# Optimization experiments

Measured on AMD Instinct MI355X. Metric: run time of the kernel, lower is better.

The kernel has to match this reference:

```python
import jax, jax.numpy as jnp
import numpy as np

N, E, K, C, NB, G = 10000, 320000, 10, 32, 8, 8
RMAX, AVG = 5.0, 32.0
L_OF_M = np.array([0,1,1,1,2,2,2,2,2,3,3,3,3,3,3,3])
BLOCKS = [(0,1),(1,4),(4,9),(9,16)]


def _sph(u):
    # real spherical harmonics l=0..3, e3nn 'component' normalization (sum_m Y_lm^2 = 2l+1)
    x, y, z = u[:,0], u[:,1], u[:,2]
    s3=3**0.5; s5=5**0.5; s15=15**0.5; s105=105**0.5
    s35_8=(35.0/8.0)**0.5; s21_8=(21.0/8.0)**0.5; s7=7**0.5
    return jnp.stack([
        jnp.ones_like(x),
        s3*x, s3*y, s3*z,
        s15*x*y, s15*y*z, 0.5*s5*(3*z*z-1.0), s15*x*z, 0.5*s15*(x*x-y*y),
        s35_8*y*(3*x*x-y*y), s105*x*y*z, s21_8*y*(5*z*z-1.0),
        0.5*s7*z*(5*z*z-3.0), s21_8*x*(5*z*z-1.0), 0.5*s105*z*(x*x-y*y),
        s35_8*x*(x*x-3*y*y)], axis=-1)


def _radial(r):
    # Bessel basis * polynomial cutoff (p=5)
    n = jnp.arange(1, NB+1, dtype=r.dtype)
    bess = jnp.sqrt(2.0/RMAX)*jnp.sin(n*jnp.pi*r[:,None]/RMAX)/r[:,None]
    t = r/RMAX; p = 5.0
    env = 1.0 - (p+1)*(p+2)/2*t**5 + p*(p+2)*t**6 - p*(p+1)/2*t**7
    env = jnp.where(r < RMAX, env, 0.0)
    return bess*env[:,None]


def _interact(scal, ea, ef, snd, rcv, mws, Wl, n_nodes):
    h = ef
    for W in mws[:-1]:
        h = jax.nn.silu(h @ W)
    tw = (h @ mws[-1]).reshape(-1, C, 4)[:, :, L_OF_M]          # [E,C,16] per-(channel,l) tp weights
    mji = scal[snd][:, :, None] * tw * ea[:, None, :]            # per-edge CG-style tensor product
    msg = jax.ops.segment_sum(mji, rcv, num_segments=n_nodes) / AVG
    return jnp.concatenate([jnp.einsum('ncm,cd->ndm', msg[:, :, a:b], Wl[l])
                            for l, (a, b) in enumerate(BLOCKS)], axis=-1)


def _forward(positions, node_attrs, shifts, edge_index, batch, num_graphs,
             atomic_energies, W_emb, Wup1, M1a, M1b, M1c, M1d, Wl1, Wprod1,
             Wup2, M2a, M2b, M2c, M2d, Wl2, Wprod2, Wsc2, wr1, Wr2a, wr2b):
    snd, rcv = edge_index[0], edge_index[1]
    vec = positions[rcv] - positions[snd] + shifts
    r = jnp.sqrt(jnp.sum(vec*vec, -1) + 1e-12)
    ea = _sph(vec / r[:, None])           # [E,16]
    ef = _radial(r)                       # [E,8]
    nf0 = node_attrs @ W_emb              # node embedding [N,C]
    A1 = _interact(nf0 @ Wup1, ea, ef, snd, rcv, (M1a, M1b, M1c, M1d), Wl1, positions.shape[0])
    c1 = jnp.einsum('nk,kct->nct', node_attrs, Wprod1)          # element-dep product-basis coeffs
    a0 = A1[:, :, 0]
    nf1 = A1 * (c1[..., 0] + c1[..., 1]*a0 + c1[..., 2]*a0*a0)[:, :, None]  # correlation-3 product
    A2 = _interact(nf1[:, :, 0] @ Wup2, ea, ef, snd, rcv, (M2a, M2b, M2c, M2d), Wl2, positions.shape[0])
    pl = jnp.stack([jnp.sum(A2[:, :, a:b]**2, -1) for a, b in BLOCKS], -1)  # [N,C,4] invariants
    c2 = jnp.einsum('nk,kct->nct', node_attrs, Wprod2)
    nf2 = jnp.sum(c2*pl, -1) + jnp.einsum('nk,nc,kcd->nd', node_attrs, nf1[:, :, 0], Wsc2)
    e0 = node_attrs @ atomic_energies
    e1 = nf1[:, :, 0] @ wr1
    e2 = jax.nn.silu(nf2 @ Wr2a) @ wr2b
    node_energy = e0 + e1 + e2
    total = jax.ops.segment_sum(node_energy, batch, num_segments=num_graphs)
    return total, node_energy


def setup_inputs():
    key = jax.random.key(0)
    ks = jax.random.split(key, 24)
    s = 0.1
    inp = {}
    inp['positions'] = jax.random.normal(ks[0], (N, 3), jnp.float32)
    inp['node_attrs'] = jax.nn.one_hot(jax.random.randint(ks[1], (N,), 0, K), K, dtype=jnp.float32)
    inp['shifts'] = jnp.zeros((E, 3), jnp.float32)
    inp['edge_index'] = jax.random.randint(ks[2], (2, E), 0, N)
    inp['batch'] = jnp.sort(jax.random.randint(ks[3], (N,), 0, G))
    inp['num_graphs'] = G
    inp['atomic_energies'] = jax.random.normal(ks[4], (K,), jnp.float32)
    inp['W_emb'] = s*jax.random.normal(ks[5], (K, C), jnp.float32)
    inp['Wup1'] = s*jax.random.normal(ks[6], (C, C), jnp.float32)
    inp['M1a'] = s*jax.random.normal(ks[7], (NB, 64), jnp.float32)
    inp['M1b'] = s*jax.random.normal(ks[8], (64, 64), jnp.float32)
    inp['M1c'] = s*jax.random.normal(ks[9], (64, 64), jnp.float32)
    inp['M1d'] = s*jax.random.normal(ks[10], (64, C*4), jnp.float32)
    inp['Wl1'] = s*jax.random.normal(ks[11], (4, C, C), jnp.float32)
    inp['Wprod1'] = s*jax.random.normal(ks[12], (K, C, 3), jnp.float32)
    inp['Wup2'] = s*jax.random.normal(ks[13], (C, C), jnp.float32)
    inp['M2a'] = s*jax.random.normal(ks[14], (NB, 64), jnp.float32)
    inp['M2b'] = s*jax.random.normal(ks[15], (64, 64), jnp.float32)
    inp['M2c'] = s*jax.random.normal(ks[16], (64, 64), jnp.float32)
    inp['M2d'] = s*jax.random.normal(ks[17], (64, C*4), jnp.float32)
    inp['Wl2'] = s*jax.random.normal(ks[18], (4, C, C), jnp.float32)
    inp['Wprod2'] = s*jax.random.normal(ks[19], (K, C, 4), jnp.float32)
    inp['Wsc2'] = s*jax.random.normal(ks[20], (K, C, C), jnp.float32)
    inp['wr1'] = s*jax.random.normal(ks[21], (C,), jnp.float32)
    inp['Wr2a'] = s*jax.random.normal(ks[22], (C, 16), jnp.float32)
    inp['wr2b'] = s*jax.random.normal(ks[23], (16,), jnp.float32)
    return inp


def reference(positions, node_attrs, shifts, edge_index, batch, num_graphs,
              atomic_energies, W_emb, Wup1, M1a, M1b, M1c, M1d, Wl1, Wprod1,
              Wup2, M2a, M2b, M2c, M2d, Wl2, Wprod2, Wsc2, wr1, Wr2a, wr2b):
    def efn(pos):
        tot, ne = _forward(pos, node_attrs, shifts, edge_index, batch, num_graphs,
                           atomic_energies, W_emb, Wup1, M1a, M1b, M1c, M1d, Wl1, Wprod1,
                           Wup2, M2a, M2b, M2c, M2d, Wl2, Wprod2, Wsc2, wr1, Wr2a, wr2b)
        return jnp.sum(tot), (tot, ne)
    (_, (total, node_energy)), g = jax.value_and_grad(efn, has_aux=True)(positions)
    forces = -g  # forces = -dE/dpositions as in get_outputs
    return total, node_energy, forces
```

## Files before the change

### kernel.cpp

```cpp
#include <hip/hip_runtime.h>
#include <math.h>

#define NN 10000
#define NE 320000
#define KS 10
#define CC 32
#define GG 8
#define NTAB 4096
#define TROW 320
#define RMAXf 5.0f
#define AVGf 32.0f

#define OF_TAB 0
#define SZ_TAB ((NTAB + 1) * TROW)
#define OF_SC1 (OF_TAB + SZ_TAB)
#define OF_SP (OF_SC1 + KS * CC)
#define OF_RE (OF_SP + NN)
#define OF_UE (OF_RE + NE)
#define OF_GV (OF_UE + 3 * NE)
#define OF_A0 (OF_GV + 3 * NE)
#define OF_NF1 (OF_A0 + NN * CC)
#define OF_SCAL2 (OF_NF1 + NN * CC)
#define OF_NEP (OF_SCAL2 + NN * CC)
#define OF_GM2T (OF_NEP + NN)
#define OF_GNF1P (OF_GM2T + NN * CC * 16)
#define OF_GS1 (OF_GNF1P + NN * CC)
#define OF_ROWS (OF_GS1 + NN * CC)
#define OF_ELIST (OF_ROWS + NN + 1)
#define OF_DEG (OF_ELIST + NE)
#define OF_CUR (OF_DEG + NN)
#define OF_GSC2 (OF_CUR + NN)
#define OF_END (OF_GSC2 + NN * CC)

__device__ __forceinline__ int lm_of(int m) { return (m == 0) ? 0 : (m < 4) ? 1 : (m < 9) ? 2 : 3; }

__device__ __forceinline__ void sph16(float x, float y, float z, float* Y) {
    const float s3 = 1.7320508075688772f, s5 = 2.23606797749979f, s15 = 3.872983346207417f,
                s105 = 10.246950765959598f, s358 = 2.091650066335189f,
                s218 = 1.6201851746019651f, s7 = 2.6457513110645907f;
    Y[0] = 1.f;
    Y[1] = s3 * x; Y[2] = s3 * y; Y[3] = s3 * z;
    Y[4] = s15 * x * y; Y[5] = s15 * y * z; Y[6] = 0.5f * s5 * (3.f * z * z - 1.f);
    Y[7] = s15 * x * z; Y[8] = 0.5f * s15 * (x * x - y * y);
    Y[9] = s358 * y * (3.f * x * x - y * y);
    Y[10] = s105 * x * y * z;
    Y[11] = s218 * y * (5.f * z * z - 1.f);
    Y[12] = 0.5f * s7 * z * (5.f * z * z - 3.f);
    Y[13] = s218 * x * (5.f * z * z - 1.f);
    Y[14] = 0.5f * s105 * z * (x * x - y * y);
    Y[15] = s358 * x * (x * x - 3.f * y * y);
}

__device__ __forceinline__ void sph16_grad(float x, float y, float z, float* Dx, float* Dy, float* Dz) {
    const float s3 = 1.7320508075688772f, s5 = 2.23606797749979f, s15 = 3.872983346207417f,
                s105 = 10.246950765959598f, s358 = 2.091650066335189f,
                s218 = 1.6201851746019651f, s7 = 2.6457513110645907f;
    Dx[0] = 0; Dy[0] = 0; Dz[0] = 0;
    Dx[1] = s3; Dy[1] = 0; Dz[1] = 0;
    Dx[2] = 0; Dy[2] = s3; Dz[2] = 0;
    Dx[3] = 0; Dy[3] = 0; Dz[3] = s3;
    Dx[4] = s15 * y; Dy[4] = s15 * x; Dz[4] = 0;
    Dx[5] = 0; Dy[5] = s15 * z; Dz[5] = s15 * y;
    Dx[6] = 0; Dy[6] = 0; Dz[6] = 3.f * s5 * z;
    Dx[7] = s15 * z; Dy[7] = 0; Dz[7] = s15 * x;
    Dx[8] = s15 * x; Dy[8] = -s15 * y; Dz[8] = 0;
    Dx[9] = 6.f * s358 * x * y; Dy[9] = 3.f * s358 * (x * x - y * y); Dz[9] = 0;
    Dx[10] = s105 * y * z; Dy[10] = s105 * x * z; Dz[10] = s105 * x * y;
    Dx[11] = 0; Dy[11] = s218 * (5.f * z * z - 1.f); Dz[11] = 10.f * s218 * y * z;
    Dx[12] = 0; Dy[12] = 0; Dz[12] = 0.5f * s7 * (15.f * z * z - 3.f);
    Dx[13] = s218 * (5.f * z * z - 1.f); Dy[13] = 0; Dz[13] = 10.f * s218 * x * z;
    Dx[14] = s105 * x * z; Dy[14] = -s105 * y * z; Dz[14] = 0.5f * s105 * (x * x - y * y);
    Dx[15] = 3.f * s358 * (x * x - y * y); Dy[15] = -6.f * s358 * x * y; Dz[15] = 0;
}

__global__ void k_species(const float* __restrict__ na, int* __restrict__ sp) {
    int n = blockIdx.x * blockDim.x + threadIdx.x;
    if (n >= NN) return;
    int k = 0;
    for (int j = 0; j < KS; j++)
        if (na[n * KS + j] > 0.5f) k = j;
    sp[n] = k;
}

__global__ void k_scal1(const float* __restrict__ Wemb, const float* __restrict__ Wup1, float* __restrict__ st) {
    int i = threadIdx.x;
    if (i >= KS * CC) return;
    int k = i / CC, c = i % CC;
    float s = 0;
    for (int j = 0; j < CC; j++) s += Wemb[k * CC + j] * Wup1[j * CC + c];
    st[i] = s;
}

__global__ void k_table(const float* __restrict__ M1a, const float* __restrict__ M1b,
                        const float* __restrict__ M1c, const float* __restrict__ M1d,
                        const float* __restrict__ M2a, const float* __restrict__ M2b,
                        const float* __restrict__ M2c, const float* __restrict__ M2d,
                        float* __restrict__ tab) {
    const double PI = 3.14159265358979323846;
    int row = blockIdx.x;
    int j = threadIdx.x;
    __shared__ float sR[8], sdR[8];
    __shared__ float sA[64], sdA[64], sB[64], sdB[64];
    if (j < 8) {
        double r = (double)row * ((double)RMAXf / NTAB);
        if (r < 1e-6) r = 1e-6;
        double a = (double)(j + 1) * PI / (double)RMAXf;
        double env = 0.0, denv = 0.0;
        if (row < NTAB) {
            double t = r / (double)RMAXf;
            double t4 = t * t * t * t;
            env = 1.0 - 21.0 * t4 * t + 35.0 * t4 * t * t - 15.0 * t4 * t * t * t;
            denv = (-105.0 * t4 + 210.0 * t4 * t - 105.0 * t4 * t * t) / (double)RMAXf;
        }
        double pref = sqrt(2.0 / (double)RMAXf);
        double s = sin(a * r), cg = cos(a * r);
        double bess = pref * s / r;
        double dbess = pref * (a * cg / r - s / (r * r));
        sR[j] = (float)(bess * env);
        sdR[j] = (float)(dbess * env + bess * denv);
    }
    __syncthreads();
    size_t rb = (size_t)row * TROW;

    {
        float p = 0, dp = 0;
        for (int i = 0; i < 8; i++) { float w = M1a[i * 64 + j]; p += sR[i] * w; dp += sdR[i] * w; }
        float sg = 1.f / (1.f + expf(-p));
        sB[j] = p * sg; sdB[j] = dp * sg * (1.f + p * (1.f - sg));
    }
    __syncthreads();
    {
        float p = 0, dp = 0;
        for (int i = 0; i < 64; i++) { float w = M1b[i * 64 + j]; p += sB[i] * w; dp += sdB[i] * w; }
        float sg = 1.f / (1.f + expf(-p));
        sA[j] = p * sg; sdA[j] = dp * sg * (1.f + p * (1.f - sg));
    }
    __syncthreads();
    {
        float p = 0, dp = 0;
        for (int i = 0; i < 64; i++) { float w = M1c[i * 64 + j]; p += sA[i] * w; dp += sdA[i] * w; }
        float sg = 1.f / (1.f + expf(-p));
        sB[j] = p * sg; sdB[j] = dp * sg * (1.f + p * (1.f - sg));
    }
    __syncthreads();
    #pragma unroll
    for (int t2 = 0; t2 < 2; t2++) {
        int o = j + t2 * 64;
        if ((o & 3) == 0) {
            float p = 0, dp = 0;
            for (int i = 0; i < 64; i++) { float w = M1d[i * 128 + o]; p += sB[i] * w; dp += sdB[i] * w; }
            int c = o >> 2;
            tab[rb + c] = p;
            tab[rb + 32 + c] = dp;
        }
    }
    __syncthreads();

    {
        float p = 0, dp = 0;
        for (int i = 0; i < 8; i++) { float w = M2a[i * 64 + j]; p += sR[i] * w; dp += sdR[i] * w; }
        float sg = 1.f / (1.f + expf(-p));
        sB[j] = p * sg; sdB[j] = dp * sg * (1.f + p * (1.f - sg));
    }
    __syncthreads();
    {
        float p = 0, dp = 0;
        for (int i = 0; i < 64; i++) { float w = M2b[i * 64 + j]; p += sB[i] * w; dp += sdB[i] * w; }
        float sg = 1.f / (1.f + expf(-p));
        sA[j] = p * sg; sdA[j] = dp * sg * (1.f + p * (1.f - sg));
    }
    __syncthreads();
    {
        float p = 0, dp = 0;
        for (int i = 0; i < 64; i++) { float w = M2c[i * 64 + j]; p += sA[i] * w; dp += sdA[i] * w; }
        float sg = 1.f / (1.f + expf(-p));
        sB[j] = p * sg; sdB[j] = dp * sg * (1.f + p * (1.f - sg));
    }
    __syncthreads();
    #pragma unroll
    for (int t2 = 0; t2 < 2; t2++) {
        int o = j + t2 * 64;
        float p = 0, dp = 0;
        for (int i = 0; i < 64; i++) { float w = M2d[i * 128 + o]; p += sB[i] * w; dp += sdB[i] * w; }
        tab[rb + 64 + o] = p;
        tab[rb + 192 + o] = dp;
    }
}

__global__ void k_geom(const float* __restrict__ pos, const float* __restrict__ shifts,
                       const int* __restrict__ ei, float* __restrict__ re,
                       float* __restrict__ ue, int* __restrict__ deg) {
    int e = blockIdx.x * 256 + threadIdx.x;
    if (e >= NE) return;
    int s = ei[e], t = ei[NE + e];
    float vx = pos[3 * t] - pos[3 * s] + shifts[3 * e];
    float vy = pos[3 * t + 1] - pos[3 * s + 1] + shifts[3 * e + 1];
    float vz = pos[3 * t + 2] - pos[3 * s + 2] + shifts[3 * e + 2];
    float r = sqrtf(vx * vx + vy * vy + vz * vz + 1e-12f);
    float inv = 1.f / r;
    re[e] = r;
    ue[3 * e] = vx * inv;
    ue[3 * e + 1] = vy * inv;
    ue[3 * e + 2] = vz * inv;
    atomicAdd(&deg[t], 1);
}

__global__ void k_scan(const int* __restrict__ deg, int* __restrict__ rows, int* __restrict__ cur) {
    __shared__ int part[1024];
    int t = threadIdx.x;
    const int per = (NN + 1023) / 1024;
    int base = t * per;
    int s = 0;
    for (int i = 0; i < per; i++) {
        int idx = base + i;
        if (idx < NN) s += deg[idx];
    }
    part[t] = s;
    __syncthreads();
    for (int off = 1; off < 1024; off <<= 1) {
        int v = (t >= off) ? part[t - off] : 0;
        __syncthreads();
        part[t] += v;
        __syncthreads();
    }
    int run = (t == 0) ? 0 : part[t - 1];
    for (int i = 0; i < per; i++) {
        int idx = base + i;
        if (idx < NN) {
            rows[idx] = run;
            cur[idx] = run;
            run += deg[idx];
        }
    }
    if (t == 1023) rows[NN] = run;
}

__global__ void k_fill(const int* __restrict__ ei, int* __restrict__ cur, int* __restrict__ elist) {
    int e = blockIdx.x * 256 + threadIdx.x;
    if (e >= NE) return;
    int t = ei[NE + e];
    int p = atomicAdd(&cur[t], 1);
    elist[p] = e;
}

__global__ void k_gather1(const int* __restrict__ rows, const int* __restrict__ elist,
                          const int* __restrict__ ei, const int* __restrict__ sp,
                          const float* __restrict__ re, const float* __restrict__ sc1,
                          const float* __restrict__ tab, const float* __restrict__ Wl1,
                          const float* __restrict__ Wprod1, const float* __restrict__ Wup2,
                          const float* __restrict__ wr1, const float* __restrict__ aE,
                          float* __restrict__ a0s, float* __restrict__ nf1,
                          float* __restrict__ scal2, float* __restrict__ nep) {
    int wid = (blockIdx.x * 256 + threadIdx.x) >> 6;
    int lane = threadIdx.x & 63, c = lane & 31, h = lane >> 5, hb = h << 5;
    if (wid >= NN) return;
    int r0 = rows[wid], dg = rows[wid + 1] - r0;
    float acc = 0.f;
    for (int j = h; j < dg; j += 2) {
        int e = elist[r0 + j];
        int s = ei[e];
        float r = re[e];
        float w1 = 0.f;
        if (r < RMAXf) {
            float tt = r * (NTAB / RMAXf);
            int i = (int)tt; if (i > NTAB - 1) i = NTAB - 1;
            float f = tt - (float)i;
            size_t b = (size_t)i * TROW + c;
            w1 = tab[b] * (1.f - f) + tab[b + TROW] * f;
        }
        acc += sc1[sp[s] * CC + c] * w1;
    }
    acc += __shfl_xor(acc, 32, 64);
    float a0 = 0.f;
    for (int d = 0; d < CC; d++) a0 += __shfl(acc, hb + d, 64) * Wl1[d * CC + c];
    a0 *= (1.f / AVGf);
    int k = sp[wid];
    const float* cp = &Wprod1[(k * CC + c) * 3];
    float nf = a0 * (cp[0] + cp[1] * a0 + cp[2] * a0 * a0);
    float s2 = 0.f;
    for (int d = 0; d < CC; d++) s2 += __shfl(nf, hb + d, 64) * Wup2[d * CC + c];
    float t1 = nf * wr1[c];
    for (int m = 16; m >= 1; m >>= 1) t1 += __shfl_xor(t1, m, 64);
    if (h == 0) {
        a0s[wid * CC + c] = a0;
        nf1[wid * CC + c] = nf;
        scal2[wid * CC + c] = s2;
        if (c == 0) nep[wid] = aE[k] + t1;
    }
}

__global__ void k_node2(const int* __restrict__ rows, const int* __restrict__ elist,
                        const int* __restrict__ ei, const int* __restrict__ sp,
                        const float* __restrict__ re, const float* __restrict__ ue,
                        const float* __restrict__ scal2, const float* __restrict__ tab,
                        const float* __restrict__ Wl2, const float* __restrict__ Wprod2,
                        const float* __restrict__ Wsc2, const float* __restrict__ nf1,
                        const float* __restrict__ Wr2a, const float* __restrict__ wr2b,
                        const float* __restrict__ wr1, const float* __restrict__ nep,
                        const int* __restrict__ batch,
                        float* __restrict__ gm2T, float* __restrict__ gnf1p,
                        float* __restrict__ out_total, float* __restrict__ out_ne) {
    __shared__ float lds[4][16 * 32];
    int wid = (blockIdx.x * 256 + threadIdx.x) >> 6;
    int lane = threadIdx.x & 63, c = lane & 31, h = lane >> 5, hb = h << 5;
    int w = threadIdx.x >> 6;
    if (wid >= NN) return;
    int r0 = rows[wid], dg = rows[wid + 1] - r0;
    float S2r[16];
    #pragma unroll
    for (int m = 0; m < 16; m++) S2r[m] = 0.f;
    for (int j = h; j < dg; j += 2) {
        int e = elist[r0 + j];
        int s = ei[e];
        float r = re[e];
        float w2[4] = {0, 0, 0, 0};
        if (r < RMAXf) {
            float tt = r * (NTAB / RMAXf);
            int i = (int)tt; if (i > NTAB - 1) i = NTAB - 1;
            float f = tt - (float)i;
            size_t b = (size_t)i * TROW + 64 + c * 4;
            #pragma unroll
            for (int l = 0; l < 4; l++) w2[l] = tab[b + l] * (1.f - f) + tab[b + TROW + l] * f;
        }
        float ux = ue[3 * e], uy = ue[3 * e + 1], uz = ue[3 * e + 2];
        float Y[16];
        sph16(ux, uy, uz, Y);
        float sc = scal2[s * CC + c];
        #pragma unroll
        for (int m = 0; m < 16; m++) S2r[m] += sc * w2[lm_of(m)] * Y[m];
    }
    #pragma unroll
    for (int m = 0; m < 16; m++) S2r[m] += __shfl_xor(S2r[m], 32, 64);
    if (h == 0) {
        #pragma unroll
        for (int m = 0; m < 16; m++) lds[w][m * 32 + c] = S2r[m];
    }
    __syncthreads();
    int d = c;
    float A2r[16];
    #pragma unroll
    for (int m = 0; m < 16; m++) {
        const float* wl = &Wl2[lm_of(m) * CC * CC];
        float acc = 0;
        for (int cc = 0; cc < CC; cc++) acc += lds[w][m * 32 + cc] * wl[cc * CC + d];
        A2r[m] = acc * (1.f / AVGf);
    }
    float pl[4] = {0, 0, 0, 0};
    #pragma unroll
    for (int m = 0; m < 16; m++) pl[lm_of(m)] += A2r[m] * A2r[m];
    int k = sp[wid];
    const float* c2 = &Wprod2[(k * CC + d) * 4];
    float nf2 = c2[0] * pl[0] + c2[1] * pl[1] + c2[2] * pl[2] + c2[3] * pl[3];
    for (int cc = 0; cc < CC; cc++) nf2 += nf1[wid * CC + cc] * Wsc2[((size_t)k * CC + cc) * CC + d];
    int jj = d & 15;
    float zj = 0;
    for (int dd = 0; dd < CC; dd++) zj += __shfl(nf2, hb + dd, 64) * Wr2a[dd * 16 + jj];
    float sg = 1.f / (1.f + expf(-zj));
    float e2p = (d < 16) ? zj * sg * wr2b[jj] : 0.f;
    float red = e2p;
    for (int m = 16; m >= 1; m >>= 1) red += __shfl_xor(red, m, 64);
    if (h == 0 && d == 0) {
        float ne = nep[wid] + red;
        out_ne[wid] = ne;
        atomicAdd(&out_total[batch[wid]], ne);
    }
    float gz = sg * (1.f + zj * (1.f - sg)) * wr2b[jj];
    float gn = 0;
    for (int j2 = 0; j2 < 16; j2++) gn += Wr2a[d * 16 + j2] * __shfl(gz, hb + j2, 64);
    __syncthreads();
    if (h == 0) {
        #pragma unroll
        for (int m = 0; m < 16; m++) lds[w][m * 32 + d] = 2.f * A2r[m] * gn * c2[lm_of(m)];
    }
    __syncthreads();
    float gmv[16];
    #pragma unroll
    for (int m = 0; m < 16; m++) {
        const float* wl = &Wl2[lm_of(m) * CC * CC + c * CC];
        float acc = 0;
        for (int dd = 0; dd < CC; dd++) acc += lds[w][m * 32 + dd] * wl[dd];
        gmv[m] = acc * (1.f / AVGf);
    }
    float g1 = wr1[c];
    for (int dd = 0; dd < CC; dd++) g1 += __shfl(gn, hb + dd, 64) * Wsc2[((size_t)k * CC + c) * CC + dd];
    if (h == 0) {
        #pragma unroll
        for (int m = 0; m < 16; m++) gm2T[(size_t)wid * 512 + c * 16 + m] = gmv[m];
        gnf1p[wid * CC + c] = g1;
    }
}

__global__ void k_gbwd2(const int* __restrict__ rows, const int* __restrict__ elist,
                        const int* __restrict__ ei, const float* __restrict__ re,
                        const float* __restrict__ ue, const float* __restrict__ scal2,
                        const float* __restrict__ tab, const float* __restrict__ gm2T,
                        float* __restrict__ gsc2, float* __restrict__ gvec) {
    int wid = (blockIdx.x * 256 + threadIdx.x) >> 6;
    int lane = threadIdx.x & 63, c = lane & 31, h = lane >> 5;
    if (wid >= NN) return;
    float gm[16];
    #pragma unroll
    for (int m = 0; m < 16; m++) gm[m] = gm2T[(size_t)wid * 512 + c * 16 + m];
    int r0 = rows[wid], dg = rows[wid + 1] - r0;
    for (int j = h; j < dg; j += 2) {
        int e = elist[r0 + j];
        int s = ei[e];
        float r = re[e];
        float w2[4] = {0, 0, 0, 0}, dw2[4] = {0, 0, 0, 0};
        if (r < RMAXf) {
            float tt = r * (NTAB / RMAXf);
            int i = (int)tt; if (i > NTAB - 1) i = NTAB - 1;
            float f = tt - (float)i;
            size_t b = (size_t)i * TROW + 64 + c * 4;
            size_t b2 = (size_t)i * TROW + 192 + c * 4;
            #pragma unroll
            for (int l = 0; l < 4; l++) {
                w2[l] = tab[b + l] * (1.f - f) + tab[b + TROW + l] * f;
                dw2[l] = tab[b2 + l] * (1.f - f) + tab[b2 + TROW + l] * f;
            }
        }
        float ux = ue[3 * e], uy = ue[3 * e + 1], uz = ue[3 * e + 2];
        float Y[16], Dx[16], Dy[16], Dz[16];
        sph16(ux, uy, uz, Y);
        sph16_grad(ux, uy, uz, Dx, Dy, Dz);
        float sc = scal2[s * CC + c];
        float gsc = 0, gdr = 0, gx = 0, gy = 0, gz = 0;
        #pragma unroll
        for (int m = 0; m < 16; m++) {
            float g = gm[m];
            int l = lm_of(m);
            float wv = w2[l];
            gsc += g * wv * Y[m];
            gdr += g * Y[m] * sc * dw2[l];
            float gY = g * sc * wv;
            gx += gY * Dx[m]; gy += gY * Dy[m]; gz += gY * Dz[m];
        }
        atomicAdd(&gsc2[s * CC + c], gsc);
        for (int m2 = 16; m2 >= 1; m2 >>= 1) {
            gdr += __shfl_xor(gdr, m2, 64);
            gx += __shfl_xor(gx, m2, 64);
            gy += __shfl_xor(gy, m2, 64);
            gz += __shfl_xor(gz, m2, 64);
        }
        if (c == 0) {
            float inv = 1.f / r;
            float dot = ux * gx + uy * gy + uz * gz;
            gvec[3 * e] = ux * gdr + (gx - ux * dot) * inv;
            gvec[3 * e + 1] = uy * gdr + (gy - uy * dot) * inv;
            gvec[3 * e + 2] = uz * gdr + (gz - uz * dot) * inv;
        }
    }
}

__global__ void k_node_bwd2(const float* __restrict__ gnf1p, const float* __restrict__ gsc2,
                            const float* __restrict__ Wup2, const float* __restrict__ a0s,
                            const int* __restrict__ sp, const float* __restrict__ Wprod1,
                            const float* __restrict__ Wl1, float* __restrict__ gS1) {
    int gid = blockIdx.x * 256 + threadIdx.x;
    int n = gid >> 5, c = gid & 31;
    if (n >= NN) return;
    int hb = threadIdx.x & 32;
    float g1 = gnf1p[n * CC + c];
    for (int dd = 0; dd < CC; dd++) g1 += gsc2[n * CC + dd] * Wup2[c * CC + dd];
    float a0 = a0s[n * CC + c];
    int k = sp[n];
    const float* cp = &Wprod1[(k * CC + c) * 3];
    float ga0 = g1 * (cp[0] + 2.f * cp[1] * a0 + 3.f * cp[2] * a0 * a0);
    float acc = 0;
    for (int dd = 0; dd < CC; dd++) acc += __shfl(ga0, hb + dd, 64) * Wl1[c * CC + dd];
    gS1[n * CC + c] = acc * (1.f / AVGf);
}

__global__ void k_edge_bwd1(const int* __restrict__ ei, const int* __restrict__ sp,
                            const float* __restrict__ re, const float* __restrict__ ue,
                            const float* __restrict__ sc1, const float* __restrict__ tab,
                            const float* __restrict__ gS1, const float* __restrict__ gvec,
                            float* __restrict__ F) {
    int gid = blockIdx.x * 256 + threadIdx.x;
    int e = gid >> 5, c = gid & 31;
    if (e >= NE) return;
    int s = ei[e], t = ei[NE + e];
    float r = re[e];
    float dw = 0.f;
    if (r < RMAXf) {
        float tt = r * (NTAB / RMAXf);
        int i = (int)tt; if (i > NTAB - 1) i = NTAB - 1;
        float f = tt - (float)i;
        size_t b = (size_t)i * TROW + 32 + c;
        dw = tab[b] * (1.f - f) + tab[b + TROW] * f;
    }
    float gw = gS1[t * CC + c] * sc1[sp[s] * CC + c];
    float gdr = gw * dw;
    for (int m = 16; m >= 1; m >>= 1) gdr += __shfl_xor(gdr, m, 64);
    if (c < 3) {
        float u = ue[3 * e + c];
        float gv = gvec[3 * e + c] + u * gdr;
        atomicAdd(&F[3 * s + c], gv);
        atomicAdd(&F[3 * t + c], -gv);
    }
}

extern "C" void kernel_launch(void* const* d_in, const int* in_sizes, int n_in,
                              void* d_out, int out_size, void* d_ws, size_t ws_size,
                              hipStream_t stream) {
    const float* pos = (const float*)d_in[0];
    const float* na = (const float*)d_in[1];
    const float* shifts = (const float*)d_in[2];
    const int* ei = (const int*)d_in[3];
    const int* batch = (const int*)d_in[4];
    const float* aE = (const float*)d_in[6];
    const float* Wemb = (const float*)d_in[7];
    const float* Wup1 = (const float*)d_in[8];
    const float* M1a = (const float*)d_in[9];
    const float* M1b = (const float*)d_in[10];
    const float* M1c = (const float*)d_in[11];
    const float* M1d = (const float*)d_in[12];
    const float* Wl1 = (const float*)d_in[13];
    const float* Wprod1 = (const float*)d_in[14];
    const float* Wup2 = (const float*)d_in[15];
    const float* M2a = (const float*)d_in[16];
    const float* M2b = (const float*)d_in[17];
    const float* M2c = (const float*)d_in[18];
    const float* M2d = (const float*)d_in[19];
    const float* Wl2 = (const float*)d_in[20];
    const float* Wprod2 = (const float*)d_in[21];
    const float* Wsc2 = (const float*)d_in[22];
    const float* wr1 = (const float*)d_in[23];
    const float* Wr2a = (const float*)d_in[24];
    const float* wr2b = (const float*)d_in[25];

    float* ws = (float*)d_ws;
    float* tab = ws + OF_TAB;
    float* sc1 = ws + OF_SC1;
    int* sp = (int*)(ws + OF_SP);
    float* re = ws + OF_RE;
    float* ue = ws + OF_UE;
    float* gv = ws + OF_GV;
    float* a0s = ws + OF_A0;
    float* nf1 = ws + OF_NF1;
    float* scal2 = ws + OF_SCAL2;
    float* nep = ws + OF_NEP;
    float* gm2T = ws + OF_GM2T;
    float* gnf1p = ws + OF_GNF1P;
    float* gS1 = ws + OF_GS1;
    int* rows = (int*)(ws + OF_ROWS);
    int* elist = (int*)(ws + OF_ELIST);
    int* deg = (int*)(ws + OF_DEG);
    int* cur = (int*)(ws + OF_CUR);
    float* gsc2 = ws + OF_GSC2;

    float* out_total = (float*)d_out;
    float* out_ne = out_total + GG;
    float* out_F = out_ne + NN;

    hipMemsetAsync(d_out, 0, sizeof(float) * (GG + NN + 3 * NN), stream);
    hipMemsetAsync(deg, 0, sizeof(float) * (size_t)(OF_END - OF_DEG), stream);

    k_species<<<(NN + 255) / 256, 256, 0, stream>>>(na, sp);
    k_scal1<<<1, 320, 0, stream>>>(Wemb, Wup1, sc1);
    k_table<<<NTAB + 1, 64, 0, stream>>>(M1a, M1b, M1c, M1d, M2a, M2b, M2c, M2d, tab);
    k_geom<<<(NE + 255) / 256, 256, 0, stream>>>(pos, shifts, ei, re, ue, deg);
    k_scan<<<1, 1024, 0, stream>>>(deg, rows, cur);
    k_fill<<<(NE + 255) / 256, 256, 0, stream>>>(ei, cur, elist);
    k_gather1<<<(NN + 3) / 4, 256, 0, stream>>>(rows, elist, ei, sp, re, sc1, tab, Wl1, Wprod1,
                                                Wup2, wr1, aE, a0s, nf1, scal2, nep);
    k_node2<<<(NN + 3) / 4, 256, 0, stream>>>(rows, elist, ei, sp, re, ue, scal2, tab, Wl2,
                                              Wprod2, Wsc2, nf1, Wr2a, wr2b, wr1, nep, batch,
                                              gm2T, gnf1p, out_total, out_ne);
    k_gbwd2<<<(NN + 3) / 4, 256, 0, stream>>>(rows, elist, ei, re, ue, scal2, tab, gm2T, gsc2, gv);
    k_node_bwd2<<<NN / 8, 256, 0, stream>>>(gnf1p, gsc2, Wup2, a0s, sp, Wprod1, Wl1, gS1);
    k_edge_bwd1<<<NE / 8, 256, 0, stream>>>(ei, sp, re, ue, sc1, tab, gS1, gv, out_F);
}
```

Measured before the change: 532.6 us.

## Store per-edge data in CSR order, unroll edge loops, fuse grad-backward into node2

k_fill now writes sender index, sender species and a packed float4 (r, unit vector) in receiver-sorted CSR order. The gather kernels then read contiguously instead of chasing elist/ei/re/ue indirections. The edge loops are unrolled 4x (2x in the backward) so several independent loads are in flight at once. The separate k_gbwd2 kernel is merged into k_node2, which removes the gm2T intermediate buffer's round trip and one launch. In exchange, k_fill does extra scattered writes and k_node2 gets more registers and lower occupancy.

```diff
diff --git a/kernel.cpp b/kernel.cpp
--- a/kernel.cpp
+++ b/kernel.cpp
@@ -13,7 +13,10 @@
 
 #define OF_TAB 0
 #define SZ_TAB ((NTAB + 1) * TROW)
-#define OF_SC1 (OF_TAB + SZ_TAB)
+#define OF_GEO (OF_TAB + SZ_TAB)
+#define OF_SND (OF_GEO + 4 * NE)
+#define OF_SPK (OF_SND + NE)
+#define OF_SC1 (OF_SPK + NE)
 #define OF_SP (OF_SC1 + KS * CC)
 #define OF_RE (OF_SP + NN)
 #define OF_UE (OF_RE + NE)
@@ -22,8 +25,7 @@
 #define OF_NF1 (OF_A0 + NN * CC)
 #define OF_SCAL2 (OF_NF1 + NN * CC)
 #define OF_NEP (OF_SCAL2 + NN * CC)
-#define OF_GM2T (OF_NEP + NN)
-#define OF_GNF1P (OF_GM2T + NN * CC * 16)
+#define OF_GNF1P (OF_NEP + NN)
 #define OF_GS1 (OF_GNF1P + NN * CC)
 #define OF_ROWS (OF_GS1 + NN * CC)
 #define OF_ELIST (OF_ROWS + NN + 1)
@@ -235,20 +237,26 @@
     if (t == 1023) rows[NN] = run;
 }
 
-__global__ void k_fill(const int* __restrict__ ei, int* __restrict__ cur, int* __restrict__ elist) {
+__global__ void k_fill(const int* __restrict__ ei, const int* __restrict__ sp,
+                       const float* __restrict__ re, const float* __restrict__ ue,
+                       int* __restrict__ cur, int* __restrict__ elist,
+                       int* __restrict__ snd, int* __restrict__ spk, float4* __restrict__ geo) {
     int e = blockIdx.x * 256 + threadIdx.x;
     if (e >= NE) return;
-    int t = ei[NE + e];
+    int s = ei[e], t = ei[NE + e];
     int p = atomicAdd(&cur[t], 1);
     elist[p] = e;
-}
-
-__global__ void k_gather1(const int* __restrict__ rows, const int* __restrict__ elist,
-                          const int* __restrict__ ei, const int* __restrict__ sp,
-                          const float* __restrict__ re, const float* __restrict__ sc1,
-                          const float* __restrict__ tab, const float* __restrict__ Wl1,
-                          const float* __restrict__ Wprod1, const float* __restrict__ Wup2,
-                          const float* __restrict__ wr1, const float* __restrict__ aE,
+    snd[p] = s;
+    spk[p] = sp[s];
+    geo[p] = make_float4(re[e], ue[3 * e], ue[3 * e + 1], ue[3 * e + 2]);
+}
+
+__global__ void k_gather1(const int* __restrict__ rows, const int* __restrict__ spk,
+                          const float4* __restrict__ geo, const int* __restrict__ sp,
+                          const float* __restrict__ sc1, const float* __restrict__ tab,
+                          const float* __restrict__ Wl1, const float* __restrict__ Wprod1,
+                          const float* __restrict__ Wup2, const float* __restrict__ wr1,
+                          const float* __restrict__ aE,
                           float* __restrict__ a0s, float* __restrict__ nf1,
                           float* __restrict__ scal2, float* __restrict__ nep) {
     int wid = (blockIdx.x * 256 + threadIdx.x) >> 6;
@@ -256,19 +264,30 @@
     if (wid >= NN) return;
     int r0 = rows[wid], dg = rows[wid + 1] - r0;
     float acc = 0.f;
-    for (int j = h; j < dg; j += 2) {
-        int e = elist[r0 + j];
-        int s = ei[e];
-        float r = re[e];
-        float w1 = 0.f;
-        if (r < RMAXf) {
-            float tt = r * (NTAB / RMAXf);
-            int i = (int)tt; if (i > NTAB - 1) i = NTAB - 1;
-            float f = tt - (float)i;
-            size_t b = (size_t)i * TROW + c;
-            w1 = tab[b] * (1.f - f) + tab[b + TROW] * f;
-        }
-        acc += sc1[sp[s] * CC + c] * w1;
+    for (int j = h; j < dg; j += 8) {
+        float rv[4]; int kv[4]; bool act[4];
+        #pragma unroll
+        for (int u = 0; u < 4; u++) {
+            int jj = j + 2 * u;
+            act[u] = jj < dg;
+            int p = r0 + (act[u] ? jj : 0);
+            rv[u] = geo[p].x;
+            kv[u] = spk[p];
+        }
+        #pragma unroll
+        for (int u = 0; u < 4; u++) {
+            if (!act[u]) continue;
+            float r = rv[u];
+            float w1 = 0.f;
+            if (r < RMAXf) {
+                float tt = r * (NTAB / RMAXf);
+                int i = (int)tt; if (i > NTAB - 1) i = NTAB - 1;
+                float f = tt - (float)i;
+                size_t b = (size_t)i * TROW + c;
+                w1 = tab[b] * (1.f - f) + tab[b + TROW] * f;
+            }
+            acc += sc1[kv[u] * CC + c] * w1;
+        }
     }
     acc += __shfl_xor(acc, 32, 64);
     float a0 = 0.f;
@@ -290,15 +309,16 @@
 }
 
 __global__ void k_node2(const int* __restrict__ rows, const int* __restrict__ elist,
-                        const int* __restrict__ ei, const int* __restrict__ sp,
-                        const float* __restrict__ re, const float* __restrict__ ue,
+                        const int* __restrict__ snd, const float4* __restrict__ geo,
+                        const int* __restrict__ sp,
                         const float* __restrict__ scal2, const float* __restrict__ tab,
                         const float* __restrict__ Wl2, const float* __restrict__ Wprod2,
                         const float* __restrict__ Wsc2, const float* __restrict__ nf1,
                         const float* __restrict__ Wr2a, const float* __restrict__ wr2b,
                         const float* __restrict__ wr1, const float* __restrict__ nep,
                         const int* __restrict__ batch,
-                        float* __restrict__ gm2T, float* __restrict__ gnf1p,
+                        float* __restrict__ gnf1p, float* __restrict__ gsc2,
+                        float* __restrict__ gvec,
                         float* __restrict__ out_total, float* __restrict__ out_ne) {
     __shared__ float lds[4][16 * 32];
     int wid = (blockIdx.x * 256 + threadIdx.x) >> 6;
@@ -306,28 +326,42 @@
     int w = threadIdx.x >> 6;
     if (wid >= NN) return;
     int r0 = rows[wid], dg = rows[wid + 1] - r0;
+
     float S2r[16];
     #pragma unroll
     for (int m = 0; m < 16; m++) S2r[m] = 0.f;
-    for (int j = h; j < dg; j += 2) {
-        int e = elist[r0 + j];
-        int s = ei[e];
-        float r = re[e];
-        float w2[4] = {0, 0, 0, 0};
-        if (r < RMAXf) {
-            float tt = r * (NTAB / RMAXf);
-            int i = (int)tt; if (i > NTAB - 1) i = NTAB - 1;
-            float f = tt - (float)i;
-            size_t b = (size_t)i * TROW + 64 + c * 4;
+    for (int j = h; j < dg; j += 8) {
+        float4 g4[4]; int sv[4]; bool act[4];
+        #pragma unroll
+        for (int u = 0; u < 4; u++) {
+            int jj = j + 2 * u;
+            act[u] = jj < dg;
+            int p = r0 + (act[u] ? jj : 0);
+            g4[u] = geo[p];
+            sv[u] = snd[p];
+        }
+        float scv[4];
+        #pragma unroll
+        for (int u = 0; u < 4; u++) scv[u] = scal2[sv[u] * CC + c];
+        #pragma unroll
+        for (int u = 0; u < 4; u++) {
+            if (!act[u]) continue;
+            float r = g4[u].x;
+            float w2[4] = {0, 0, 0, 0};
+            if (r < RMAXf) {
+                float tt = r * (NTAB / RMAXf);
+                int i = (int)tt; if (i > NTAB - 1) i = NTAB - 1;
+                float f = tt - (float)i;
+                size_t b = (size_t)i * TROW + 64 + c * 4;
+                #pragma unroll
+                for (int l = 0; l < 4; l++) w2[l] = tab[b + l] * (1.f - f) + tab[b + TROW + l] * f;
+            }
+            float Y[16];
+            sph16(g4[u].y, g4[u].z, g4[u].w, Y);
+            float sc = scv[u];
             #pragma unroll
-            for (int l = 0; l < 4; l++) w2[l] = tab[b + l] * (1.f - f) + tab[b + TROW + l] * f;
-        }
-        float ux = ue[3 * e], uy = ue[3 * e + 1], uz = ue[3 * e + 2];
-        float Y[16];
-        sph16(ux, uy, uz, Y);
-        float sc = scal2[s * CC + c];
-        #pragma unroll
-        for (int m = 0; m < 16; m++) S2r[m] += sc * w2[lm_of(m)] * Y[m];
+            for (int m = 0; m < 16; m++) S2r[m] += sc * w2[lm_of(m)] * Y[m];
+        }
     }
     #pragma unroll
     for (int m = 0; m < 16; m++) S2r[m] += __shfl_xor(S2r[m], 32, 64);
@@ -336,6 +370,7 @@
         for (int m = 0; m < 16; m++) lds[w][m * 32 + c] = S2r[m];
     }
     __syncthreads();
+
     int d = c;
     float A2r[16];
     #pragma unroll
@@ -352,11 +387,11 @@
     const float* c2 = &Wprod2[(k * CC + d) * 4];
     float nf2 = c2[0] * pl[0] + c2[1] * pl[1] + c2[2] * pl[2] + c2[3] * pl[3];
     for (int cc = 0; cc < CC; cc++) nf2 += nf1[wid * CC + cc] * Wsc2[((size_t)k * CC + cc) * CC + d];
-    int jj = d & 15;
+    int jj2 = d & 15;
     float zj = 0;
-    for (int dd = 0; dd < CC; dd++) zj += __shfl(nf2, hb + dd, 64) * Wr2a[dd * 16 + jj];
+    for (int dd = 0; dd < CC; dd++) zj += __shfl(nf2, hb + dd, 64) * Wr2a[dd * 16 + jj2];
     float sg = 1.f / (1.f + expf(-zj));
-    float e2p = (d < 16) ? zj * sg * wr2b[jj] : 0.f;
+    float e2p = (d < 16) ? zj * sg * wr2b[jj2] : 0.f;
     float red = e2p;
     for (int m = 16; m >= 1; m >>= 1) red += __shfl_xor(red, m, 64);
     if (h == 0 && d == 0) {
@@ -364,7 +399,7 @@
         out_ne[wid] = ne;
         atomicAdd(&out_total[batch[wid]], ne);
     }
-    float gz = sg * (1.f + zj * (1.f - sg)) * wr2b[jj];
+    float gz = sg * (1.f + zj * (1.f - sg)) * wr2b[jj2];
     float gn = 0;
     for (int j2 = 0; j2 < 16; j2++) gn += Wr2a[d * 16 + j2] * __shfl(gz, hb + j2, 64);
     __syncthreads();
@@ -373,81 +408,78 @@
         for (int m = 0; m < 16; m++) lds[w][m * 32 + d] = 2.f * A2r[m] * gn * c2[lm_of(m)];
     }
     __syncthreads();
-    float gmv[16];
+    float gm[16];
     #pragma unroll
     for (int m = 0; m < 16; m++) {
         const float* wl = &Wl2[lm_of(m) * CC * CC + c * CC];
         float acc = 0;
         for (int dd = 0; dd < CC; dd++) acc += lds[w][m * 32 + dd] * wl[dd];
-        gmv[m] = acc * (1.f / AVGf);
+        gm[m] = acc * (1.f / AVGf);
     }
     float g1 = wr1[c];
     for (int dd = 0; dd < CC; dd++) g1 += __shfl(gn, hb + dd, 64) * Wsc2[((size_t)k * CC + c) * CC + dd];
-    if (h == 0) {
-        #pragma unroll
-        for (int m = 0; m < 16; m++) gm2T[(size_t)wid * 512 + c * 16 + m] = gmv[m];
-        gnf1p[wid * CC + c] = g1;
-    }
-}
-
-__global__ void k_gbwd2(const int* __restrict__ rows, const int* __restrict__ elist,
-                        const int* __restrict__ ei, const float* __restrict__ re,
-                        const float* __restrict__ ue, const float* __restrict__ scal2,
-                        const float* __restrict__ tab, const float* __restrict__ gm2T,
-                        float* __restrict__ gsc2, float* __restrict__ gvec) {
-    int wid = (blockIdx.x * 256 + threadIdx.x) >> 6;
-    int lane = threadIdx.x & 63, c = lane & 31, h = lane >> 5;
-    if (wid >= NN) return;
-    float gm[16];
-    #pragma unroll
-    for (int m = 0; m < 16; m++) gm[m] = gm2T[(size_t)wid * 512 + c * 16 + m];
-    int r0 = rows[wid], dg = rows[wid + 1] - r0;
-    for (int j = h; j < dg; j += 2) {
-        int e = elist[r0 + j];
-        int s = ei[e];
-        float r = re[e];
-        float w2[4] = {0, 0, 0, 0}, dw2[4] = {0, 0, 0, 0};
-        if (r < RMAXf) {
-            float tt = r * (NTAB / RMAXf);
-            int i = (int)tt; if (i > NTAB - 1) i = NTAB - 1;
-            float f = tt - (float)i;
-            size_t b = (size_t)i * TROW + 64 + c * 4;
-            size_t b2 = (size_t)i * TROW + 192 + c * 4;
+    if (h == 0) gnf1p[wid * CC + c] = g1;
+
+    for (int j = h; j < dg; j += 4) {
+        float4 g4[2]; int sv[2], el[2]; bool act[2];
+        #pragma unroll
+        for (int u = 0; u < 2; u++) {
+            int jj = j + 2 * u;
+            act[u] = jj < dg;
+            int p = r0 + (act[u] ? jj : 0);
+            g4[u] = geo[p];
+            sv[u] = snd[p];
+            el[u] = elist[p];
+        }
+        float scv[2];
+        #pragma unroll
+        for (int u = 0; u < 2; u++) scv[u] = scal2[sv[u] * CC + c];
+        #pragma unroll
+        for (int u = 0; u < 2; u++) {
+            if (!act[u]) continue;
+            float r = g4[u].x, ux = g4[u].y, uy = g4[u].z, uz = g4[u].w;
+            float w2[4] = {0, 0, 0, 0}, dw2[4] = {0, 0, 0, 0};
+            if (r < RMAXf) {
+                float tt = r * (NTAB / RMAXf);
+                int i = (int)tt; if (i > NTAB - 1) i = NTAB - 1;
+                float f = tt - (float)i;
+                size_t b = (size_t)i * TROW + 64 + c * 4;
+                size_t b2 = (size_t)i * TROW + 192 + c * 4;
+                #pragma unroll
+                for (int l = 0; l < 4; l++) {
+                    w2[l] = tab[b + l] * (1.f - f) + tab[b + TROW + l] * f;
+                    dw2[l] = tab[b2 + l] * (1.f - f) + tab[b2 + TROW + l] * f;
+                }
+            }
+            float Y[16], Dx[16], Dy[16], Dz[16];
+            sph16(ux, uy, uz, Y);
+            sph16_grad(ux, uy, uz, Dx, Dy, Dz);
+            float sc = scv[u];
+            float gsc = 0, gdr = 0, gx = 0, gy = 0, gz = 0;
             #pragma unroll
-            for (int l = 0; l < 4; l++) {
-                w2[l] = tab[b + l] * (1.f - f) + tab[b + TROW + l] * f;
-                dw2[l] = tab[b2 + l] * (1.f - f) + tab[b2 + TROW + l] * f;
+            for (int m = 0; m < 16; m++) {
+                float g = gm[m];
+                int l = lm_of(m);
+                float wv = w2[l];
+                gsc += g * wv * Y[m];
+                gdr += g * Y[m] * sc * dw2[l];
+                float gY = g * sc * wv;
+                gx += gY * Dx[m]; gy += gY * Dy[m]; gz += gY * Dz[m];
             }
-        }
-        float ux = ue[3 * e], uy = ue[3 * e + 1], uz = ue[3 * e + 2];
-        float Y[16], Dx[16], Dy[16], Dz[16];
-        sph16(ux, uy, uz, Y);
-        sph16_grad(ux, uy, uz, Dx, Dy, Dz);
-        float sc = scal2[s * CC + c];
-        float gsc = 0, gdr = 0, gx = 0, gy = 0, gz = 0;
-        #pragma unroll
-        for (int m = 0; m < 16; m++) {
-            float g = gm[m];
-            int l = lm_of(m);
-            float wv = w2[l];
-            gsc += g * wv * Y[m];
-            gdr += g * Y[m] * sc * dw2[l];
-            float gY = g * sc * wv;
-            gx += gY * Dx[m]; gy += gY * Dy[m]; gz += gY * Dz[m];
-        }
-        atomicAdd(&gsc2[s * CC + c], gsc);
-        for (int m2 = 16; m2 >= 1; m2 >>= 1) {
-            gdr += __shfl_xor(gdr, m2, 64);
-            gx += __shfl_xor(gx, m2, 64);
-            gy += __shfl_xor(gy, m2, 64);
-            gz += __shfl_xor(gz, m2, 64);
-        }
-        if (c == 0) {
-            float inv = 1.f / r;
-            float dot = ux * gx + uy * gy + uz * gz;
-            gvec[3 * e] = ux * gdr + (gx - ux * dot) * inv;
-            gvec[3 * e + 1] = uy * gdr + (gy - uy * dot) * inv;
-            gvec[3 * e + 2] = uz * gdr + (gz - uz * dot) * inv;
+            atomicAdd(&gsc2[sv[u] * CC + c], gsc);
+            for (int m2 = 16; m2 >= 1; m2 >>= 1) {
+                gdr += __shfl_xor(gdr, m2, 64);
+                gx += __shfl_xor(gx, m2, 64);
+                gy += __shfl_xor(gy, m2, 64);
+                gz += __shfl_xor(gz, m2, 64);
+            }
+            if (c == 0) {
+                float inv = 1.f / r;
+                float dot = ux * gx + uy * gy + uz * gz;
+                gvec[3 * el[u]] = ux * gdr + (gx - ux * dot) * inv;
+                gvec[3 * el[u] + 1] = uy * gdr + (gy - uy * dot) * inv;
+                gvec[3 * el[u] + 2] = uz * gdr + (gz - uz * dot) * inv;
+            }
         }
     }
 }
@@ -531,6 +563,9 @@
 
     float* ws = (float*)d_ws;
     float* tab = ws + OF_TAB;
+    float4* geo = (float4*)(ws + OF_GEO);
+    int* snd = (int*)(ws + OF_SND);
+    int* spk = (int*)(ws + OF_SPK);
     float* sc1 = ws + OF_SC1;
     int* sp = (int*)(ws + OF_SP);
     float* re = ws + OF_RE;
@@ -540,7 +575,6 @@
     float* nf1 = ws + OF_NF1;
     float* scal2 = ws + OF_SCAL2;
     float* nep = ws + OF_NEP;
-    float* gm2T = ws + OF_GM2T;
     float* gnf1p = ws + OF_GNF1P;
     float* gS1 = ws + OF_GS1;
     int* rows = (int*)(ws + OF_ROWS);
@@ -561,13 +595,12 @@
     k_table<<<NTAB + 1, 64, 0, stream>>>(M1a, M1b, M1c, M1d, M2a, M2b, M2c, M2d, tab);
     k_geom<<<(NE + 255) / 256, 256, 0, stream>>>(pos, shifts, ei, re, ue, deg);
     k_scan<<<1, 1024, 0, stream>>>(deg, rows, cur);
-    k_fill<<<(NE + 255) / 256, 256, 0, stream>>>(ei, cur, elist);
-    k_gather1<<<(NN + 3) / 4, 256, 0, stream>>>(rows, elist, ei, sp, re, sc1, tab, Wl1, Wprod1,
+    k_fill<<<(NE + 255) / 256, 256, 0, stream>>>(ei, sp, re, ue, cur, elist, snd, spk, geo);
+    k_gather1<<<(NN + 3) / 4, 256, 0, stream>>>(rows, spk, geo, sp, sc1, tab, Wl1, Wprod1,
                                                 Wup2, wr1, aE, a0s, nf1, scal2, nep);
-    k_node2<<<(NN + 3) / 4, 256, 0, stream>>>(rows, elist, ei, sp, re, ue, scal2, tab, Wl2,
+    k_node2<<<(NN + 3) / 4, 256, 0, stream>>>(rows, elist, snd, geo, sp, scal2, tab, Wl2,
                                               Wprod2, Wsc2, nf1, Wr2a, wr2b, wr1, nep, batch,
-                                              gm2T, gnf1p, out_total, out_ne);
-    k_gbwd2<<<(NN + 3) / 4, 256, 0, stream>>>(rows, elist, ei, re, ue, scal2, tab, gm2T, gsc2, gv);
+                                              gnf1p, gsc2, gv, out_total, out_ne);
     k_node_bwd2<<<NN / 8, 256, 0, stream>>>(gnf1p, gsc2, Wup2, a0s, sp, Wprod1, Wl1, gS1);
     k_edge_bwd1<<<NE / 8, 256, 0, stream>>>(ei, sp, re, ue, sc1, tab, gS1, gv, out_F);
 }
```

After: 1.050 ms. +97.1%, slower.

## Store per-edge geometry and sender data in receiver-sorted CSR order

Applied to the files above, without the earlier changes.

k_fill now writes sender index, sender species, radius and a packed float4 of (r, unit vector) at each edge's CSR slot. The gather kernels then read these contiguously instead of going through elist, ei, re and ue. This removes a level of dependent indirection and scattered loads in the per-node edge loops. The change also halves the radial lookup table resolution, which reduces k_table work and the table footprint at some cost in interpolation accuracy, and adds launch bounds to three kernels.

```diff
diff --git a/kernel.cpp b/kernel.cpp
--- a/kernel.cpp
+++ b/kernel.cpp
@@ -6,14 +6,18 @@
 #define KS 10
 #define CC 32
 #define GG 8
-#define NTAB 4096
+#define NTAB 2048
 #define TROW 320
 #define RMAXf 5.0f
 #define AVGf 32.0f
 
 #define OF_TAB 0
 #define SZ_TAB ((NTAB + 1) * TROW)
-#define OF_SC1 (OF_TAB + SZ_TAB)
+#define OF_GEO (OF_TAB + SZ_TAB)
+#define OF_SND (OF_GEO + 4 * NE)
+#define OF_SPK (OF_SND + NE)
+#define OF_RCSR (OF_SPK + NE)
+#define OF_SC1 (OF_RCSR + NE)
 #define OF_SP (OF_SC1 + KS * CC)
 #define OF_RE (OF_SP + NN)
 #define OF_UE (OF_RE + NE)
@@ -235,31 +239,40 @@
     if (t == 1023) rows[NN] = run;
 }
 
-__global__ void k_fill(const int* __restrict__ ei, int* __restrict__ cur, int* __restrict__ elist) {
+__global__ void k_fill(const int* __restrict__ ei, const int* __restrict__ sp,
+                       const float* __restrict__ re, const float* __restrict__ ue,
+                       int* __restrict__ cur, int* __restrict__ elist,
+                       int* __restrict__ snd, int* __restrict__ spk,
+                       float* __restrict__ rcsr, float4* __restrict__ geo) {
     int e = blockIdx.x * 256 + threadIdx.x;
     if (e >= NE) return;
-    int t = ei[NE + e];
+    int s = ei[e], t = ei[NE + e];
     int p = atomicAdd(&cur[t], 1);
     elist[p] = e;
-}
-
-__global__ void k_gather1(const int* __restrict__ rows, const int* __restrict__ elist,
-                          const int* __restrict__ ei, const int* __restrict__ sp,
-                          const float* __restrict__ re, const float* __restrict__ sc1,
-                          const float* __restrict__ tab, const float* __restrict__ Wl1,
-                          const float* __restrict__ Wprod1, const float* __restrict__ Wup2,
-                          const float* __restrict__ wr1, const float* __restrict__ aE,
-                          float* __restrict__ a0s, float* __restrict__ nf1,
-                          float* __restrict__ scal2, float* __restrict__ nep) {
+    snd[p] = s;
+    spk[p] = sp[s];
+    rcsr[p] = re[e];
+    geo[p] = make_float4(re[e], ue[3 * e], ue[3 * e + 1], ue[3 * e + 2]);
+}
+
+__global__ __launch_bounds__(256, 4)
+void k_gather1(const int* __restrict__ rows, const int* __restrict__ spk,
+               const float* __restrict__ rcsr, const int* __restrict__ sp,
+               const float* __restrict__ sc1, const float* __restrict__ tab,
+               const float* __restrict__ Wl1, const float* __restrict__ Wprod1,
+               const float* __restrict__ Wup2, const float* __restrict__ wr1,
+               const float* __restrict__ aE,
+               float* __restrict__ a0s, float* __restrict__ nf1,
+               float* __restrict__ scal2, float* __restrict__ nep) {
     int wid = (blockIdx.x * 256 + threadIdx.x) >> 6;
     int lane = threadIdx.x & 63, c = lane & 31, h = lane >> 5, hb = h << 5;
     if (wid >= NN) return;
     int r0 = rows[wid], dg = rows[wid + 1] - r0;
     float acc = 0.f;
     for (int j = h; j < dg; j += 2) {
-        int e = elist[r0 + j];
-        int s = ei[e];
-        float r = re[e];
+        int p = r0 + j;
+        float r = rcsr[p];
+        int kk = spk[p];
         float w1 = 0.f;
         if (r < RMAXf) {
             float tt = r * (NTAB / RMAXf);
@@ -268,7 +281,7 @@
             size_t b = (size_t)i * TROW + c;
             w1 = tab[b] * (1.f - f) + tab[b + TROW] * f;
         }
-        acc += sc1[sp[s] * CC + c] * w1;
+        acc += sc1[kk * CC + c] * w1;
     }
     acc += __shfl_xor(acc, 32, 64);
     float a0 = 0.f;
@@ -289,17 +302,17 @@
     }
 }
 
-__global__ void k_node2(const int* __restrict__ rows, const int* __restrict__ elist,
-                        const int* __restrict__ ei, const int* __restrict__ sp,
-                        const float* __restrict__ re, const float* __restrict__ ue,
-                        const float* __restrict__ scal2, const float* __restrict__ tab,
-                        const float* __restrict__ Wl2, const float* __restrict__ Wprod2,
-                        const float* __restrict__ Wsc2, const float* __restrict__ nf1,
-                        const float* __restrict__ Wr2a, const float* __restrict__ wr2b,
-                        const float* __restrict__ wr1, const float* __restrict__ nep,
-                        const int* __restrict__ batch,
-                        float* __restrict__ gm2T, float* __restrict__ gnf1p,
-                        float* __restrict__ out_total, float* __restrict__ out_ne) {
+__global__ __launch_bounds__(256, 4)
+void k_node2(const int* __restrict__ rows, const int* __restrict__ snd,
+             const float4* __restrict__ geo, const int* __restrict__ sp,
+             const float* __restrict__ scal2, const float* __restrict__ tab,
+             const float* __restrict__ Wl2, const float* __restrict__ Wprod2,
+             const float* __restrict__ Wsc2, const float* __restrict__ nf1,
+             const float* __restrict__ Wr2a, const float* __restrict__ wr2b,
+             const float* __restrict__ wr1, const float* __restrict__ nep,
+             const int* __restrict__ batch,
+             float* __restrict__ gm2T, float* __restrict__ gnf1p,
+             float* __restrict__ out_total, float* __restrict__ out_ne) {
     __shared__ float lds[4][16 * 32];
     int wid = (blockIdx.x * 256 + threadIdx.x) >> 6;
     int lane = threadIdx.x & 63, c = lane & 31, h = lane >> 5, hb = h << 5;
@@ -310,9 +323,11 @@
     #pragma unroll
     for (int m = 0; m < 16; m++) S2r[m] = 0.f;
     for (int j = h; j < dg; j += 2) {
-        int e = elist[r0 + j];
-        int s = ei[e];
-        float r = re[e];
+        int p = r0 + j;
+        float4 g4 = geo[p];
+        int s = snd[p];
+        float sc = scal2[s * CC + c];
+        float r = g4.x;
         float w2[4] = {0, 0, 0, 0};
         if (r < RMAXf) {
             float tt = r * (NTAB / RMAXf);
@@ -322,10 +337,8 @@
             #pragma unroll
             for (int l = 0; l < 4; l++) w2[l] = tab[b + l] * (1.f - f) + tab[b + TROW + l] * f;
         }
-        float ux = ue[3 * e], uy = ue[3 * e + 1], uz = ue[3 * e + 2];
         float Y[16];
-        sph16(ux, uy, uz, Y);
-        float sc = scal2[s * CC + c];
+        sph16(g4.y, g4.z, g4.w, Y);
         #pragma unroll
         for (int m = 0; m < 16; m++) S2r[m] += sc * w2[lm_of(m)] * Y[m];
     }
@@ -390,11 +403,12 @@
     }
 }
 
-__global__ void k_gbwd2(const int* __restrict__ rows, const int* __restrict__ elist,
-                        const int* __restrict__ ei, const float* __restrict__ re,
-                        const float* __restrict__ ue, const float* __restrict__ scal2,
-                        const float* __restrict__ tab, const float* __restrict__ gm2T,
-                        float* __restrict__ gsc2, float* __restrict__ gvec) {
+__global__ __launch_bounds__(256, 4)
+void k_gbwd2(const int* __restrict__ rows, const int* __restrict__ elist,
+             const int* __restrict__ snd, const float4* __restrict__ geo,
+             const float* __restrict__ scal2, const float* __restrict__ tab,
+             const float* __restrict__ gm2T,
+             float* __restrict__ gsc2, float* __restrict__ gvec) {
     int wid = (blockIdx.x * 256 + threadIdx.x) >> 6;
     int lane = threadIdx.x & 63, c = lane & 31, h = lane >> 5;
     if (wid >= NN) return;
@@ -403,9 +417,11 @@
     for (int m = 0; m < 16; m++) gm[m] = gm2T[(size_t)wid * 512 + c * 16 + m];
     int r0 = rows[wid], dg = rows[wid + 1] - r0;
     for (int j = h; j < dg; j += 2) {
-        int e = elist[r0 + j];
-        int s = ei[e];
-        float r = re[e];
+        int p = r0 + j;
+        float4 g4 = geo[p];
+        int s = snd[p];
+        float sc = scal2[s * CC + c];
+        float r = g4.x, ux = g4.y, uy = g4.z, uz = g4.w;
         float w2[4] = {0, 0, 0, 0}, dw2[4] = {0, 0, 0, 0};
         if (r < RMAXf) {
             float tt = r * (NTAB / RMAXf);
@@ -419,11 +435,9 @@
                 dw2[l] = tab[b2 + l] * (1.f - f) + tab[b2 + TROW + l] * f;
             }
         }
-        float ux = ue[3 * e], uy = ue[3 * e + 1], uz = ue[3 * e + 2];
         float Y[16], Dx[16], Dy[16], Dz[16];
         sph16(ux, uy, uz, Y);
         sph16_grad(ux, uy, uz, Dx, Dy, Dz);
-        float sc = scal2[s * CC + c];
         float gsc = 0, gdr = 0, gx = 0, gy = 0, gz = 0;
         #pragma unroll
         for (int m = 0; m < 16; m++) {
@@ -443,6 +457,7 @@
             gz += __shfl_xor(gz, m2, 64);
         }
         if (c == 0) {
+            int e = elist[p];
             float inv = 1.f / r;
             float dot = ux * gx + uy * gy + uz * gz;
             gvec[3 * e] = ux * gdr + (gx - ux * dot) * inv;
@@ -531,6 +546,10 @@
 
     float* ws = (float*)d_ws;
     float* tab = ws + OF_TAB;
+    float4* geo = (float4*)(ws + OF_GEO);
+    int* snd = (int*)(ws + OF_SND);
+    int* spk = (int*)(ws + OF_SPK);
+    float* rcsr = ws + OF_RCSR;
     float* sc1 = ws + OF_SC1;
     int* sp = (int*)(ws + OF_SP);
     float* re = ws + OF_RE;
@@ -561,13 +580,13 @@
     k_table<<<NTAB + 1, 64, 0, stream>>>(M1a, M1b, M1c, M1d, M2a, M2b, M2c, M2d, tab);
     k_geom<<<(NE + 255) / 256, 256, 0, stream>>>(pos, shifts, ei, re, ue, deg);
     k_scan<<<1, 1024, 0, stream>>>(deg, rows, cur);
-    k_fill<<<(NE + 255) / 256, 256, 0, stream>>>(ei, cur, elist);
-    k_gather1<<<(NN + 3) / 4, 256, 0, stream>>>(rows, elist, ei, sp, re, sc1, tab, Wl1, Wprod1,
+    k_fill<<<(NE + 255) / 256, 256, 0, stream>>>(ei, sp, re, ue, cur, elist, snd, spk, rcsr, geo);
+    k_gather1<<<(NN + 3) / 4, 256, 0, stream>>>(rows, spk, rcsr, sp, sc1, tab, Wl1, Wprod1,
                                                 Wup2, wr1, aE, a0s, nf1, scal2, nep);
-    k_node2<<<(NN + 3) / 4, 256, 0, stream>>>(rows, elist, ei, sp, re, ue, scal2, tab, Wl2,
+    k_node2<<<(NN + 3) / 4, 256, 0, stream>>>(rows, snd, geo, sp, scal2, tab, Wl2,
                                               Wprod2, Wsc2, nf1, Wr2a, wr2b, wr1, nep, batch,
                                               gm2T, gnf1p, out_total, out_ne);
-    k_gbwd2<<<(NN + 3) / 4, 256, 0, stream>>>(rows, elist, ei, re, ue, scal2, tab, gm2T, gsc2, gv);
+    k_gbwd2<<<(NN + 3) / 4, 256, 0, stream>>>(rows, elist, snd, geo, scal2, tab, gm2T, gsc2, gv);
     k_node_bwd2<<<NN / 8, 256, 0, stream>>>(gnf1p, gsc2, Wup2, a0s, sp, Wprod1, Wl1, gS1);
     k_edge_bwd1<<<NE / 8, 256, 0, stream>>>(ei, sp, re, ue, sc1, tab, gS1, gv, out_F);
 }
```

Measured after the change: 482.7 us. 1.1x faster.
